# Kernel tuning notes

Measured on AMD Instinct MI355X. Metric: run time of the kernel, lower is better.

## Reference

```python
import jax, jax.numpy as jnp
import numpy as np

H, W = 32, 64          # img_size
NB = 4                 # fno_blocks
SCALE = 0.02


def setup_inputs() -> dict:
    key = jax.random.key(0)
    ks = jax.random.split(key, 8)
    B, N, C = 16, H * W, 768
    BS = C // NB
    x = jax.random.normal(ks[0], (B, N, C), dtype=jnp.float32)
    w1 = SCALE * jax.random.normal(ks[1], (2, NB, BS, BS), dtype=jnp.float32)
    b1 = SCALE * jax.random.normal(ks[2], (2, NB, BS), dtype=jnp.float32)
    w2 = SCALE * jax.random.normal(ks[3], (2, NB, BS, BS), dtype=jnp.float32)
    b2 = SCALE * jax.random.normal(ks[4], (2, NB, BS), dtype=jnp.float32)
    # Conv1d(C, C, kernel_size=1) == per-token linear layer over channels
    bias_w = jax.random.normal(ks[5], (C, C), dtype=jnp.float32) / np.sqrt(C)
    bias_b = jax.random.normal(ks[6], (C,), dtype=jnp.float32) * 0.01
    return {"x": x, "w1": w1, "b1": b1, "w2": w2, "b2": b2,
            "bias_w": bias_w, "bias_b": bias_b}


def _mul(a, w):
    # block-diagonal matmul: a [..., NB, BS], w [NB, BS, BS]
    return jnp.einsum('...bd,bdk->...bk', a, w)


def reference(x, w1, b1, w2, b2, bias_w, bias_b):
    B, N, C = x.shape
    BS = C // NB
    # Conv1d kernel-size-1 bias path
    bias = x @ bias_w.T + bias_b
    # spatial FFT
    xf = jnp.fft.rfftn(x.reshape(B, H, W, C), axes=(1, 2), norm='ortho')
    xf = xf.reshape(B, H, W // 2 + 1, NB, BS)
    xr, xi = xf.real, xf.imag
    # layer 1 (complex block-diag matmul + bias, ReLU on real/imag separately)
    r1 = jax.nn.relu(_mul(xr, w1[0]) - _mul(xi, w1[1]) + b1[0])
    i1 = jax.nn.relu(_mul(xr, w1[1]) + _mul(xi, w1[0]) + b1[1])
    # layer 2 -- NOTE: imag part uses the *updated* real part, matching the
    # original torch code's in-place reassignment order.
    r2 = _mul(r1, w2[0]) - _mul(i1, w2[1]) + b2[0]
    i2 = _mul(r2, w2[1]) + _mul(i1, w2[0]) + b2[1]
    xc = jax.lax.complex(r2, i2).reshape(B, H, W // 2 + 1, C)
    out = jnp.fft.irfftn(xc, s=(H, W), axes=(1, 2), norm='ortho')
    return out.reshape(B, N, C) + bias
```

## Files before the change

### kernel.cpp

```cpp
#include <hip/hip_runtime.h>
#include <hip/hip_bf16.h>
#include <stdint.h>

#define BB 16
#define HH 32
#define WW 64
#define CC 768
#define W2C 33
#define ROWW (2*CC)

typedef __bf16 bf16x8 __attribute__((ext_vector_type(8)));
typedef float f32x4 __attribute__((ext_vector_type(4)));

__device__ __forceinline__ unsigned short f2bf(float f) {
  __hip_bfloat16 h = __float2bfloat16(f);
  return __builtin_bit_cast(unsigned short, h);
}
__device__ __forceinline__ float bf2f(unsigned short u) {
  union { unsigned int i; float f; } x;
  x.i = ((unsigned int)u) << 16;
  return x.f;
}

__device__ __forceinline__ void g2l16(const void* g, void* l) {
  __builtin_amdgcn_global_load_lds((const __attribute__((address_space(1))) unsigned int*)g,
                                   (__attribute__((address_space(3))) unsigned int*)l,
                                   16, 0, 0);
}

#define WAITVM(n) asm volatile("s_waitcnt vmcnt(" #n ")" ::: "memory")
#define LGKM0() asm volatile("s_waitcnt lgkmcnt(0)" ::: "memory")
#define MEMFENCE() asm volatile("" ::: "memory")

__device__ __host__ constexpr int brevc(int x, int bits) {
  int r = 0;
  for (int i = 0; i < bits; ++i) r |= ((x >> i) & 1) << (bits - 1 - i);
  return r;
}

constexpr double TPI = 6.283185307179586476925286766559;
constexpr double tsin_(double x) {
  double t = x, s = x, x2 = x * x;
  for (int i = 1; i < 14; ++i) { t *= -x2 / (double)((2 * i) * (2 * i + 1)); s += t; }
  return s;
}
constexpr double tcos_(double x) {
  double t = 1.0, s = 1.0, x2 = x * x;
  for (int i = 1; i < 14; ++i) { t *= -x2 / (double)((2 * i - 1) * (2 * i)); s += t; }
  return s;
}
struct Tw64 { float c[64]; float s[64]; };
constexpr Tw64 mk_tw() {
  Tw64 r{};
  for (int k = 0; k < 64; ++k) {
    int q = k >> 4, m = k & 15;
    double a = (TPI / 64.0) * m;
    double cq = tcos_(a), sq = tsin_(a);
    double c, s;
    if (q == 0)      { c =  cq; s =  sq; }
    else if (q == 1) { c = -sq; s =  cq; }
    else if (q == 2) { c = -cq; s = -sq; }
    else             { c =  sq; s = -cq; }
    r.c[k] = (float)c;
    r.s[k] = (float)(-s);
  }
  return r;
}
constexpr Tw64 TW = mk_tw();

template<int N, bool INV>
__device__ __forceinline__ void fft_reg(float2 (&v)[N]) {
  constexpr int LOG2N = (N == 64) ? 6 : 5;
#pragma unroll
  for (int s = 0; s < LOG2N; ++s) {
    const int len = N >> s;
    const int half = len >> 1;
    const int tstep = 64 / len;
#pragma unroll
    for (int i = 0; i < N; i += len) {
#pragma unroll
      for (int j = 0; j < half; ++j) {
        float2 u = v[i + j];
        float2 t = v[i + j + half];
        float sr = u.x + t.x, si = u.y + t.y;
        float dr = u.x - t.x, di = u.y - t.y;
        float wr = TW.c[j * tstep];
        float wi = INV ? -TW.s[j * tstep] : TW.s[j * tstep];
        v[i + j] = make_float2(sr, si);
        v[i + j + half] = make_float2(dr * wr - di * wi, dr * wi + di * wr);
      }
    }
  }
}

__global__ __launch_bounds__(128) void fft_fwd_w(const float* __restrict__ x,
                                                 ushort2* __restrict__ yw) {
  __shared__ __align__(16) float xs[32][128];
  const int t = threadIdx.x;
  const int bh = blockIdx.x;
  const int c0 = blockIdx.y * 128;
  const float* xrow = x + (size_t)bh * (WW * CC) + c0;
  const int rg = t >> 5;
  const int lc = (t & 31) * 4;
  float2 v[32];
#pragma unroll
  for (int half = 0; half < 2; ++half) {
    if (half) __syncthreads();
    float4 f[8];
#pragma unroll
    for (int it = 0; it < 8; ++it)
      f[it] = *(const float4*)(xrow + (size_t)(half * 32 + it * 4 + rg) * CC + lc);
#pragma unroll
    for (int it = 0; it < 8; ++it)
      *(float4*)&xs[it * 4 + rg][lc] = f[it];
    __syncthreads();
#pragma unroll
    for (int n = 0; n < 16; ++n)
      v[half * 16 + n] = make_float2(xs[2 * n][t], xs[2 * n + 1][t]);
  }
  fft_reg<32, false>(v);
  ushort2* yp = yw + (size_t)bh * (W2C * CC) + c0 + t;
  {
    float2 Z0 = v[0];
    yp[0] = make_ushort2(f2bf(Z0.x + Z0.y), f2bf(0.f));
    yp[(size_t)32 * CC] = make_ushort2(f2bf(Z0.x - Z0.y), f2bf(0.f));
  }
#pragma unroll
  for (int k = 1; k < 32; ++k) {
    float2 Zk = v[brevc(k, 5)];
    float2 Zm = v[brevc(32 - k, 5)];
    float Er = 0.5f * (Zk.x + Zm.x), Ei = 0.5f * (Zk.y - Zm.y);
    float Odr = 0.5f * (Zk.y + Zm.y), Odi = -0.5f * (Zk.x - Zm.x);
    float wx = TW.c[k], wy = TW.s[k];
    float Xr = Er + wx * Odr - wy * Odi;
    float Xi = Ei + wx * Odi + wy * Odr;
    yp[(size_t)k * CC] = make_ushort2(f2bf(Xr), f2bf(Xi));
  }
}

__global__ __launch_bounds__(256) void fused_bias_ffth(
    const float* __restrict__ x, const unsigned short* __restrict__ bwb,
    const float* __restrict__ bb, unsigned short* __restrict__ biasout,
    const ushort2* __restrict__ yw, unsigned short* __restrict__ xf) {
  __shared__ __align__(16) unsigned short As[2][128 * 32];
  __shared__ __align__(16) unsigned short Bs[2][128 * 32];
  const int gid = blockIdx.x;
  bool isg; int idx;
  if (gid < 3072) { isg = (gid & 1) == 0; idx = gid >> 1; }
  else            { isg = false; idx = 1536 + (gid - 3072); }

  if (isg) {
    constexpr int K = 768, NT = 24, LDAF = 768;
    const int t = threadIdx.x;
    const int bx = idx & 255, by = idx >> 8;
    const size_t m0 = (size_t)bx * 128;
    const int n0 = by * 128;
    const float* Ap = x + m0 * LDAF;
    const unsigned short* Bp = bwb + (size_t)n0 * K;
    const int lane = t & 63, wave = t >> 6;
    const int lr = lane & 15, quad = lane >> 4;
    const int wm = (wave >> 1) * 64, wn = (wave & 1) * 64;
    const int row = t >> 2, sl = t & 3;
    const int kb = (sl ^ ((row >> 1) & 3)) * 8;
    const int swzf = (lr >> 1) & 3;
    f32x4 acc[4][4] = {};
    float4 a0, a1, a2, a3;

#define LDA4(k0_) do { \
    const float* ga_ = Ap + (size_t)row * LDAF + ((k0_) + kb); \
    a0 = *(const float4*)ga_; a1 = *(const float4*)(ga_ + 4); \
    const float* gc_ = ga_ + (size_t)64 * LDAF; \
    a2 = *(const float4*)gc_; a3 = *(const float4*)(gc_ + 4); \
  } while (0)
#define STB(k0_, s_) do { \
    const unsigned short* gb_ = Bp + (size_t)row * K + ((k0_) + kb); \
    g2l16(gb_, &Bs[s_][row * 32 + sl * 8]); \
    g2l16(gb_ + (size_t)64 * K, &Bs[s_][(row + 64) * 32 + sl * 8]); \
  } while (0)
#define WRA(s_) do { \
    union { bf16x8 v; unsigned short u[8]; } p0_, p1_; \
    p0_.u[0] = f2bf(a0.x); p0_.u[1] = f2bf(a0.y); p0_.u[2] = f2bf(a0.z); p0_.u[3] = f2bf(a0.w); \
    p0_.u[4] = f2bf(a1.x); p0_.u[5] = f2bf(a1.y); p0_.u[6] = f2bf(a1.z); p0_.u[7] = f2bf(a1.w); \
    p1_.u[0] = f2bf(a2.x); p1_.u[1] = f2bf(a2.y); p1_.u[2] = f2bf(a2.z); p1_.u[3] = f2bf(a2.w); \
    p1_.u[4] = f2bf(a3.x); p1_.u[5] = f2bf(a3.y); p1_.u[6] = f2bf(a3.z); p1_.u[7] = f2bf(a3.w); \
    *(bf16x8*)&As[s_][row * 32 + sl * 8] = p0_.v; \
    *(bf16x8*)&As[s_][(row + 64) * 32 + sl * 8] = p1_.v; \
  } while (0)

    LDA4(0); STB(0, 0);
    WRA(0);
    WAITVM(0); LGKM0();
    MEMFENCE(); __builtin_amdgcn_s_barrier(); MEMFENCE();
    int cur = 0;
    for (int tt = 0; tt < NT; ++tt) {
      if (tt + 1 < NT) { LDA4((tt + 1) * 32); STB((tt + 1) * 32, cur ^ 1); }
      bf16x8 af[4], bfr[4];
#pragma unroll
      for (int mi = 0; mi < 4; ++mi)
        af[mi] = *(const bf16x8*)&As[cur][(wm + mi * 16 + lr) * 32 + ((quad ^ swzf) * 8)];
#pragma unroll
      for (int ni = 0; ni < 4; ++ni)
        bfr[ni] = *(const bf16x8*)&Bs[cur][(wn + ni * 16 + lr) * 32 + ((quad ^ swzf) * 8)];
      __builtin_amdgcn_s_setprio(1);
#pragma unroll
      for (int mi = 0; mi < 4; ++mi)
#pragma unroll
        for (int ni = 0; ni < 4; ++ni)
          acc[mi][ni] = __builtin_amdgcn_mfma_f32_16x16x32_bf16(af[mi], bfr[ni], acc[mi][ni], 0, 0, 0);
      __builtin_amdgcn_s_setprio(0);
      if (tt + 1 < NT) {
        WRA(cur ^ 1);
        WAITVM(0); LGKM0();
        MEMFENCE(); __builtin_amdgcn_s_barrier(); MEMFENCE();
        cur ^= 1;
      }
    }
#undef LDA4
#undef STB
#undef WRA

#pragma unroll
    for (int mi = 0; mi < 4; ++mi) {
      const size_t mrow = m0 + wm + mi * 16 + quad * 4;
#pragma unroll
      for (int ni = 0; ni < 4; ++ni) {
        const int ncol = n0 + wn + ni * 16 + lr;
        const float bv = bb[ncol];
#pragma unroll
        for (int r = 0; r < 4; ++r)
          biasout[(mrow + r) * (size_t)768 + ncol] = f2bf(acc[mi][ni][r] + bv);
      }
    }
  } else {
    const int bk = idx - (idx / 528) * 528;
    const int cy = idx / 528;
    const int b = bk / W2C, kw = bk - b * W2C;
    const int c = cy * 256 + threadIdx.x;
    const ushort2* yp = yw + ((size_t)b * HH * W2C + kw) * CC + c;
    float2 v[32];
#pragma unroll
    for (int h = 0; h < 32; ++h) {
      ushort2 u = yp[(size_t)h * (W2C * CC)];
      v[h] = make_float2(bf2f(u.x), bf2f(u.y));
    }
    fft_reg<32, false>(v);
    const int nb = c / 192, cc = c - nb * 192;
    ushort2* xp = (ushort2*)(xf + (size_t)nb * 384 + 2 * cc);
    const float s = 0.022097086912079608f;
#pragma unroll
    for (int kh = 0; kh < 32; ++kh) {
      float2 z = v[brevc(kh, 5)];
      size_t m = ((size_t)b * HH + kh) * W2C + kw;
      xp[m * (ROWW / 2)] = make_ushort2(f2bf(z.x * s), f2bf(z.y * s));
    }
  }
}

__global__ __launch_bounds__(256) void fft_inv_h(const unsigned short* __restrict__ r2,
                                                 ushort2* __restrict__ g) {
  const int bk = blockIdx.x;
  const int b = bk / W2C, kw = bk - b * W2C;
  const int c = blockIdx.y * 256 + threadIdx.x;
  const int nb = c / 192, cc = c - nb * 192;
  const ushort2* rp = (const ushort2*)(r2 + (size_t)nb * 384 + 2 * cc);
  float2 v[32];
#pragma unroll
  for (int kh = 0; kh < 32; ++kh) {
    size_t m = ((size_t)b * HH + kh) * W2C + kw;
    ushort2 u = rp[m * (ROWW / 2)];
    v[kh] = make_float2(bf2f(u.x), bf2f(u.y));
  }
  fft_reg<32, true>(v);
  ushort2* gp = g + ((size_t)b * HH * W2C + kw) * CC + c;
#pragma unroll
  for (int h = 0; h < 32; ++h) {
    float2 z = v[brevc(h, 5)];
    gp[(size_t)h * (W2C * CC)] = make_ushort2(f2bf(z.x), f2bf(z.y));
  }
}

__global__ __launch_bounds__(128) void fft_inv_w(const ushort2* __restrict__ g,
                                                 const unsigned short* __restrict__ biasb,
                                                 float* __restrict__ out) {
  __shared__ __align__(16) float ys[32][128];
  const int t = threadIdx.x;
  const int bh = blockIdx.x;
  const int c0 = blockIdx.y * 128;
  const ushort2* gp = g + (size_t)bh * (W2C * CC) + c0 + t;
  float2 v[32];
  {
    float X0 = bf2f(gp[0].x);
    float X32 = bf2f(gp[(size_t)32 * CC].x);
    v[0] = make_float2(0.5f * (X0 + X32), 0.5f * (X0 - X32));
  }
#pragma unroll
  for (int k = 1; k < 32; ++k) {
    ushort2 uk = gp[(size_t)k * CC];
    ushort2 um = gp[(size_t)(32 - k) * CC];
    float2 Xk = make_float2(bf2f(uk.x), bf2f(uk.y));
    float2 Xm = make_float2(bf2f(um.x), bf2f(um.y));
    float Ar = 0.5f * (Xk.x + Xm.x), Ai = 0.5f * (Xk.y - Xm.y);
    float Dr = 0.5f * (Xk.x - Xm.x), Di = 0.5f * (Xk.y + Xm.y);
    float wx = TW.c[k], wy = TW.s[k];
    float Br = wx * Dr + wy * Di;
    float Bi = wx * Di - wy * Dr;
    v[k] = make_float2(Ar - Bi, Ai + Br);
  }
  fft_reg<32, true>(v);
  const float s2 = 0.04419417382415922f;
  float* orow = out + (size_t)bh * (WW * CC) + c0;
  const unsigned short* brow = biasb + (size_t)bh * (WW * CC) + c0;
  const int rg = t >> 5;
  const int lc = (t & 31) * 4;
#pragma unroll
  for (int half = 0; half < 2; ++half) {
    if (half) __syncthreads();
    ushort4 b4[8];
#pragma unroll
    for (int it = 0; it < 8; ++it)
      b4[it] = *(const ushort4*)(brow + (size_t)(half * 32 + it * 4 + rg) * CC + lc);
#pragma unroll
    for (int n = 0; n < 16; ++n) {
      float2 z = v[brevc(half * 16 + n, 5)];
      ys[2 * n][t] = z.x * s2;
      ys[2 * n + 1][t] = z.y * s2;
    }
    __syncthreads();
#pragma unroll
    for (int it = 0; it < 8; ++it) {
      const int w = half * 32 + it * 4 + rg;
      float4 f = *(const float4*)&ys[it * 4 + rg][lc];
      f.x += bf2f(b4[it].x); f.y += bf2f(b4[it].y);
      f.z += bf2f(b4[it].z); f.w += bf2f(b4[it].w);
      *(float4*)(orow + (size_t)w * CC + lc) = f;
    }
  }
}

template<bool RELU, bool OBF>
__global__ __launch_bounds__(256) void gemm_bt(
    const unsigned short* __restrict__ A, int lda, int aZ,
    const unsigned short* __restrict__ Bw, int K, int bZ,
    const float* __restrict__ bias, int biasZ,
    void* __restrict__ outp, int ldo, int oZ) {
  __shared__ __align__(16) unsigned short As[2][128 * 32];
  __shared__ __align__(16) unsigned short Bs[2][128 * 32];
  const int t = threadIdx.x;
  const int z = blockIdx.z;
  const size_t m0 = (size_t)blockIdx.x * 128;
  const int n0 = blockIdx.y * 128;
  const unsigned short* Ap = A + m0 * lda + (size_t)z * aZ;
  const unsigned short* Bp = Bw + (size_t)n0 * K + (size_t)z * bZ;
  const int lane = t & 63, wave = t >> 6;
  const int lr = lane & 15, quad = lane >> 4;
  const int wm = (wave >> 1) * 64, wn = (wave & 1) * 64;
  const int row = t >> 2;
  const int sl = t & 3;
  const int kb = (sl ^ ((row >> 1) & 3)) * 8;
  const int swzf = (lr >> 1) & 3;
  const int NT = K >> 5;
  f32x4 acc[4][4] = {};

#define STG(k0_, s_) do { \
    const unsigned short* ga_ = Ap + (size_t)row * lda + ((k0_) + kb); \
    g2l16(ga_, &As[s_][row * 32 + sl * 8]); \
    g2l16(ga_ + (size_t)64 * lda, &As[s_][(row + 64) * 32 + sl * 8]); \
    const unsigned short* gb_ = Bp + (size_t)row * K + ((k0_) + kb); \
    g2l16(gb_, &Bs[s_][row * 32 + sl * 8]); \
    g2l16(gb_ + (size_t)64 * K, &Bs[s_][(row + 64) * 32 + sl * 8]); \
  } while (0)

  STG(0, 0);
  WAITVM(0);
  MEMFENCE(); __builtin_amdgcn_s_barrier(); MEMFENCE();
  int cur = 0;
  for (int tt = 0; tt < NT; ++tt) {
    if (tt + 1 < NT) STG((tt + 1) * 32, cur ^ 1);
    bf16x8 af[4], bfr[4];
#pragma unroll
    for (int mi = 0; mi < 4; ++mi)
      af[mi] = *(const bf16x8*)&As[cur][(wm + mi * 16 + lr) * 32 + ((quad ^ swzf) * 8)];
#pragma unroll
    for (int ni = 0; ni < 4; ++ni)
      bfr[ni] = *(const bf16x8*)&Bs[cur][(wn + ni * 16 + lr) * 32 + ((quad ^ swzf) * 8)];
    __builtin_amdgcn_s_setprio(1);
#pragma unroll
    for (int mi = 0; mi < 4; ++mi)
#pragma unroll
      for (int ni = 0; ni < 4; ++ni)
        acc[mi][ni] = __builtin_amdgcn_mfma_f32_16x16x32_bf16(af[mi], bfr[ni], acc[mi][ni], 0, 0, 0);
    __builtin_amdgcn_s_setprio(0);
    if (tt + 1 < NT) {
      WAITVM(0);
      MEMFENCE(); __builtin_amdgcn_s_barrier(); MEMFENCE();
      cur ^= 1;
    }
  }
#undef STG

#pragma unroll
  for (int mi = 0; mi < 4; ++mi) {
    const size_t mrow = m0 + wm + mi * 16 + quad * 4;
#pragma unroll
    for (int ni = 0; ni < 4; ++ni) {
      const int ncol = n0 + wn + ni * 16 + lr;
      const float bv = bias[z * biasZ + ncol];
#pragma unroll
      for (int r = 0; r < 4; ++r) {
        float vv = acc[mi][ni][r] + bv;
        if (RELU) vv = fmaxf(vv, 0.f);
        const size_t off = (mrow + r) * (size_t)ldo + (size_t)z * oZ + ncol;
        if (OBF) ((unsigned short*)outp)[off] = f2bf(vv);
        else ((float*)outp)[off] = vv;
      }
    }
  }
}

__global__ __launch_bounds__(256) void prep_all(
    const float* __restrict__ bw, unsigned short* __restrict__ bwb,
    const float* __restrict__ w1, const float* __restrict__ b1,
    unsigned short* __restrict__ w1t, float* __restrict__ bias1,
    const float* __restrict__ w2, const float* __restrict__ b2,
    unsigned short* __restrict__ w2t, float* __restrict__ bias2) {
  const int gid = blockIdx.x;
  const int t = threadIdx.x;
  if (gid < 576) {
    const size_t i = ((size_t)gid * 256 + t) * 4;
    float4 v = *(const float4*)(bw + i);
    *(ushort4*)(bwb + i) = make_ushort4(f2bf(v.x), f2bf(v.y), f2bf(v.z), f2bf(v.w));
  } else if (gid < 576 + 2304) {
    const int idx = (gid - 576) * 256 + t;
    const int nb = idx / (384 * 384);
    const int rem = idx - nb * (384 * 384);
    const int n = rem / 384, k = rem - (rem / 384) * 384;
    const bool khi = k >= 192, nhi = n >= 192;
    const int kk = khi ? k - 192 : k, nn = nhi ? n - 192 : n;
    float val;
    if (!khi && !nhi)      val =  w1[((0 * 4 + nb) * 192 + kk) * 192 + nn];
    else if (khi && !nhi)  val = -w1[((1 * 4 + nb) * 192 + kk) * 192 + nn];
    else if (!khi && nhi)  val =  w1[((1 * 4 + nb) * 192 + kk) * 192 + nn];
    else                   val =  w1[((0 * 4 + nb) * 192 + kk) * 192 + nn];
    const int k2 = 2 * kk + (khi ? 1 : 0);
    const int n2 = 2 * nn + (nhi ? 1 : 0);
    w1t[((size_t)nb * 384 + n2) * 384 + k2] = f2bf(val);
    if (k == 0)
      bias1[nb * 384 + n2] = nhi ? b1[(1 * 4 + nb) * 192 + nn] : b1[(0 * 4 + nb) * 192 + nn];
  } else {
    const int idx = (gid - 2880) * 256 + t;
    const int nb = idx / (384 * 384);
    const int rem = idx - nb * (384 * 384);
    const int k = rem / 384, n = rem - (rem / 384) * 384;
    const bool khi = k >= 192, nhi = n >= 192;
    const int kk = khi ? k - 192 : k, nn = nhi ? n - 192 : n;
    float val;
    if (!khi && !nhi) {
      val = w2[((0 * 4 + nb) * 192 + kk) * 192 + nn];
    } else if (khi && !nhi) {
      val = -w2[((1 * 4 + nb) * 192 + kk) * 192 + nn];
    } else if (!khi && nhi) {
      float s = 0.f;
      for (int d = 0; d < 192; ++d)
        s += w2[((0 * 4 + nb) * 192 + kk) * 192 + d] * w2[((1 * 4 + nb) * 192 + d) * 192 + nn];
      val = s;
    } else {
      float s = 0.f;
      for (int d = 0; d < 192; ++d)
        s += w2[((1 * 4 + nb) * 192 + kk) * 192 + d] * w2[((1 * 4 + nb) * 192 + d) * 192 + nn];
      val = w2[((0 * 4 + nb) * 192 + kk) * 192 + nn] - s;
    }
    const int k2 = 2 * kk + (khi ? 1 : 0);
    const int n2 = 2 * nn + (nhi ? 1 : 0);
    w2t[((size_t)nb * 384 + n2) * 384 + k2] = f2bf(val);
    if (k == 0) {
      float bv;
      if (!nhi) {
        bv = b2[(0 * 4 + nb) * 192 + nn];
      } else {
        float s = 0.f;
        for (int d = 0; d < 192; ++d)
          s += b2[(0 * 4 + nb) * 192 + d] * w2[((1 * 4 + nb) * 192 + d) * 192 + nn];
        bv = b2[(1 * 4 + nb) * 192 + nn] + s;
      }
      bias2[nb * 384 + n2] = bv;
    }
  }
}

extern "C" void kernel_launch(void* const* d_in, const int* in_sizes, int n_in,
                              void* d_out, int out_size, void* d_ws, size_t ws_size,
                              hipStream_t stream) {
  (void)in_sizes; (void)n_in; (void)out_size; (void)ws_size;
  const float* x  = (const float*)d_in[0];
  const float* w1 = (const float*)d_in[1];
  const float* b1 = (const float*)d_in[2];
  const float* w2 = (const float*)d_in[3];
  const float* b2 = (const float*)d_in[4];
  const float* bw = (const float*)d_in[5];
  const float* bb = (const float*)d_in[6];
  float* out = (float*)d_out;

  char* p = (char*)d_ws;
  unsigned short* buf1 = (unsigned short*)p; p += 51904512;
  unsigned short* buf2 = (unsigned short*)p; p += 51904512;
  unsigned short* buf3 = (unsigned short*)p; p += 51904512;
  unsigned short* bwb  = (unsigned short*)p; p += 1179648;
  unsigned short* w1t  = (unsigned short*)p; p += 1179648;
  unsigned short* w2t  = (unsigned short*)p; p += 1179648;
  float* bias1 = (float*)p; p += 6144;
  float* bias2 = (float*)p; p += 6144;

  prep_all<<<5184, 256, 0, stream>>>(bw, bwb, w1, b1, w1t, bias1, w2, b2, w2t, bias2);
  fft_fwd_w<<<dim3(BB * HH, 6), 128, 0, stream>>>(x, (ushort2*)buf1);
  fused_bias_ffth<<<3120, 256, 0, stream>>>(x, bwb, bb, buf3, (const ushort2*)buf1, buf2);
  gemm_bt<true, true><<<dim3(132, 3, 4), 256, 0, stream>>>(
      buf2, ROWW, 384, w1t, 384, 384 * 384, bias1, 384, buf1, ROWW, 384);
  gemm_bt<false, true><<<dim3(132, 3, 4), 256, 0, stream>>>(
      buf1, ROWW, 384, w2t, 384, 384 * 384, bias2, 384, buf2, ROWW, 384);
  fft_inv_h<<<dim3(BB * W2C, 3), 256, 0, stream>>>(buf2, (ushort2*)buf1);
  fft_inv_w<<<dim3(BB * HH, 6), 128, 0, stream>>>((const ushort2*)buf1, buf3, out);
}
```

Baseline: 500.2 us.

## Unfuse bias GEMM from H-FFT and enlarge GEMM tiles to 256-wide

Splits the fused bias-GEMM/forward-H-FFT kernel back into two separate launches. It also grows the GEMM tiles: the spectral GEMMs now use 256x128 tiles (8x4 MFMA accumulators per wave) and the bias GEMM uses 128x256 tiles. The larger tiles cut redundant operand loads from global memory. The cost is higher register and LDS use per block, which lowers occupancy and leaves fewer blocks (e.g. 792 spectral-GEMM blocks instead of 1584). It also gives up the concurrency the fused kernel had between compute-bound GEMM blocks and memory-bound FFT blocks.

```diff
diff --git a/kernel.cpp b/kernel.cpp
--- a/kernel.cpp
+++ b/kernel.cpp
@@ -138,121 +138,27 @@
   }
 }
 
-__global__ __launch_bounds__(256) void fused_bias_ffth(
-    const float* __restrict__ x, const unsigned short* __restrict__ bwb,
-    const float* __restrict__ bb, unsigned short* __restrict__ biasout,
-    const ushort2* __restrict__ yw, unsigned short* __restrict__ xf) {
-  __shared__ __align__(16) unsigned short As[2][128 * 32];
-  __shared__ __align__(16) unsigned short Bs[2][128 * 32];
-  const int gid = blockIdx.x;
-  bool isg; int idx;
-  if (gid < 3072) { isg = (gid & 1) == 0; idx = gid >> 1; }
-  else            { isg = false; idx = 1536 + (gid - 3072); }
-
-  if (isg) {
-    constexpr int K = 768, NT = 24, LDAF = 768;
-    const int t = threadIdx.x;
-    const int bx = idx & 255, by = idx >> 8;
-    const size_t m0 = (size_t)bx * 128;
-    const int n0 = by * 128;
-    const float* Ap = x + m0 * LDAF;
-    const unsigned short* Bp = bwb + (size_t)n0 * K;
-    const int lane = t & 63, wave = t >> 6;
-    const int lr = lane & 15, quad = lane >> 4;
-    const int wm = (wave >> 1) * 64, wn = (wave & 1) * 64;
-    const int row = t >> 2, sl = t & 3;
-    const int kb = (sl ^ ((row >> 1) & 3)) * 8;
-    const int swzf = (lr >> 1) & 3;
-    f32x4 acc[4][4] = {};
-    float4 a0, a1, a2, a3;
-
-#define LDA4(k0_) do { \
-    const float* ga_ = Ap + (size_t)row * LDAF + ((k0_) + kb); \
-    a0 = *(const float4*)ga_; a1 = *(const float4*)(ga_ + 4); \
-    const float* gc_ = ga_ + (size_t)64 * LDAF; \
-    a2 = *(const float4*)gc_; a3 = *(const float4*)(gc_ + 4); \
-  } while (0)
-#define STB(k0_, s_) do { \
-    const unsigned short* gb_ = Bp + (size_t)row * K + ((k0_) + kb); \
-    g2l16(gb_, &Bs[s_][row * 32 + sl * 8]); \
-    g2l16(gb_ + (size_t)64 * K, &Bs[s_][(row + 64) * 32 + sl * 8]); \
-  } while (0)
-#define WRA(s_) do { \
-    union { bf16x8 v; unsigned short u[8]; } p0_, p1_; \
-    p0_.u[0] = f2bf(a0.x); p0_.u[1] = f2bf(a0.y); p0_.u[2] = f2bf(a0.z); p0_.u[3] = f2bf(a0.w); \
-    p0_.u[4] = f2bf(a1.x); p0_.u[5] = f2bf(a1.y); p0_.u[6] = f2bf(a1.z); p0_.u[7] = f2bf(a1.w); \
-    p1_.u[0] = f2bf(a2.x); p1_.u[1] = f2bf(a2.y); p1_.u[2] = f2bf(a2.z); p1_.u[3] = f2bf(a2.w); \
-    p1_.u[4] = f2bf(a3.x); p1_.u[5] = f2bf(a3.y); p1_.u[6] = f2bf(a3.z); p1_.u[7] = f2bf(a3.w); \
-    *(bf16x8*)&As[s_][row * 32 + sl * 8] = p0_.v; \
-    *(bf16x8*)&As[s_][(row + 64) * 32 + sl * 8] = p1_.v; \
-  } while (0)
-
-    LDA4(0); STB(0, 0);
-    WRA(0);
-    WAITVM(0); LGKM0();
-    MEMFENCE(); __builtin_amdgcn_s_barrier(); MEMFENCE();
-    int cur = 0;
-    for (int tt = 0; tt < NT; ++tt) {
-      if (tt + 1 < NT) { LDA4((tt + 1) * 32); STB((tt + 1) * 32, cur ^ 1); }
-      bf16x8 af[4], bfr[4];
-#pragma unroll
-      for (int mi = 0; mi < 4; ++mi)
-        af[mi] = *(const bf16x8*)&As[cur][(wm + mi * 16 + lr) * 32 + ((quad ^ swzf) * 8)];
-#pragma unroll
-      for (int ni = 0; ni < 4; ++ni)
-        bfr[ni] = *(const bf16x8*)&Bs[cur][(wn + ni * 16 + lr) * 32 + ((quad ^ swzf) * 8)];
-      __builtin_amdgcn_s_setprio(1);
-#pragma unroll
-      for (int mi = 0; mi < 4; ++mi)
-#pragma unroll
-        for (int ni = 0; ni < 4; ++ni)
-          acc[mi][ni] = __builtin_amdgcn_mfma_f32_16x16x32_bf16(af[mi], bfr[ni], acc[mi][ni], 0, 0, 0);
-      __builtin_amdgcn_s_setprio(0);
-      if (tt + 1 < NT) {
-        WRA(cur ^ 1);
-        WAITVM(0); LGKM0();
-        MEMFENCE(); __builtin_amdgcn_s_barrier(); MEMFENCE();
-        cur ^= 1;
-      }
-    }
-#undef LDA4
-#undef STB
-#undef WRA
-
-#pragma unroll
-    for (int mi = 0; mi < 4; ++mi) {
-      const size_t mrow = m0 + wm + mi * 16 + quad * 4;
-#pragma unroll
-      for (int ni = 0; ni < 4; ++ni) {
-        const int ncol = n0 + wn + ni * 16 + lr;
-        const float bv = bb[ncol];
-#pragma unroll
-        for (int r = 0; r < 4; ++r)
-          biasout[(mrow + r) * (size_t)768 + ncol] = f2bf(acc[mi][ni][r] + bv);
-      }
-    }
-  } else {
-    const int bk = idx - (idx / 528) * 528;
-    const int cy = idx / 528;
-    const int b = bk / W2C, kw = bk - b * W2C;
-    const int c = cy * 256 + threadIdx.x;
-    const ushort2* yp = yw + ((size_t)b * HH * W2C + kw) * CC + c;
-    float2 v[32];
-#pragma unroll
-    for (int h = 0; h < 32; ++h) {
-      ushort2 u = yp[(size_t)h * (W2C * CC)];
-      v[h] = make_float2(bf2f(u.x), bf2f(u.y));
-    }
-    fft_reg<32, false>(v);
-    const int nb = c / 192, cc = c - nb * 192;
-    ushort2* xp = (ushort2*)(xf + (size_t)nb * 384 + 2 * cc);
-    const float s = 0.022097086912079608f;
-#pragma unroll
-    for (int kh = 0; kh < 32; ++kh) {
-      float2 z = v[brevc(kh, 5)];
-      size_t m = ((size_t)b * HH + kh) * W2C + kw;
-      xp[m * (ROWW / 2)] = make_ushort2(f2bf(z.x * s), f2bf(z.y * s));
-    }
+__global__ __launch_bounds__(256) void fft_fwd_h(const ushort2* __restrict__ yw,
+                                                 unsigned short* __restrict__ xf) {
+  const int bk = blockIdx.x;
+  const int b = bk / W2C, kw = bk - b * W2C;
+  const int c = blockIdx.y * 256 + threadIdx.x;
+  const ushort2* yp = yw + ((size_t)b * HH * W2C + kw) * CC + c;
+  float2 v[32];
+#pragma unroll
+  for (int h = 0; h < 32; ++h) {
+    ushort2 u = yp[(size_t)h * (W2C * CC)];
+    v[h] = make_float2(bf2f(u.x), bf2f(u.y));
+  }
+  fft_reg<32, false>(v);
+  const int nb = c / 192, cc = c - nb * 192;
+  ushort2* xp = (ushort2*)(xf + (size_t)nb * 384 + 2 * cc);
+  const float s = 0.022097086912079608f;
+#pragma unroll
+  for (int kh = 0; kh < 32; ++kh) {
+    float2 z = v[brevc(kh, 5)];
+    size_t m = ((size_t)b * HH + kh) * W2C + kw;
+    xp[m * (ROWW / 2)] = make_ushort2(f2bf(z.x * s), f2bf(z.y * s));
   }
 }
 
@@ -337,34 +243,36 @@
   }
 }
 
-template<bool RELU, bool OBF>
-__global__ __launch_bounds__(256) void gemm_bt(
+template<bool RELU>
+__global__ __launch_bounds__(256) void gemm_spec(
     const unsigned short* __restrict__ A, int lda, int aZ,
     const unsigned short* __restrict__ Bw, int K, int bZ,
     const float* __restrict__ bias, int biasZ,
-    void* __restrict__ outp, int ldo, int oZ) {
-  __shared__ __align__(16) unsigned short As[2][128 * 32];
+    unsigned short* __restrict__ outp, int ldo, int oZ) {
+  __shared__ __align__(16) unsigned short As[2][256 * 32];
   __shared__ __align__(16) unsigned short Bs[2][128 * 32];
   const int t = threadIdx.x;
   const int z = blockIdx.z;
-  const size_t m0 = (size_t)blockIdx.x * 128;
+  const size_t m0 = (size_t)blockIdx.x * 256;
   const int n0 = blockIdx.y * 128;
   const unsigned short* Ap = A + m0 * lda + (size_t)z * aZ;
   const unsigned short* Bp = Bw + (size_t)n0 * K + (size_t)z * bZ;
   const int lane = t & 63, wave = t >> 6;
   const int lr = lane & 15, quad = lane >> 4;
-  const int wm = (wave >> 1) * 64, wn = (wave & 1) * 64;
+  const int wm = (wave >> 1) * 128, wn = (wave & 1) * 64;
   const int row = t >> 2;
   const int sl = t & 3;
   const int kb = (sl ^ ((row >> 1) & 3)) * 8;
   const int swzf = (lr >> 1) & 3;
   const int NT = K >> 5;
-  f32x4 acc[4][4] = {};
+  f32x4 acc[8][4] = {};
 
 #define STG(k0_, s_) do { \
     const unsigned short* ga_ = Ap + (size_t)row * lda + ((k0_) + kb); \
     g2l16(ga_, &As[s_][row * 32 + sl * 8]); \
     g2l16(ga_ + (size_t)64 * lda, &As[s_][(row + 64) * 32 + sl * 8]); \
+    g2l16(ga_ + (size_t)128 * lda, &As[s_][(row + 128) * 32 + sl * 8]); \
+    g2l16(ga_ + (size_t)192 * lda, &As[s_][(row + 192) * 32 + sl * 8]); \
     const unsigned short* gb_ = Bp + (size_t)row * K + ((k0_) + kb); \
     g2l16(gb_, &Bs[s_][row * 32 + sl * 8]); \
     g2l16(gb_ + (size_t)64 * K, &Bs[s_][(row + 64) * 32 + sl * 8]); \
@@ -376,16 +284,16 @@
   int cur = 0;
   for (int tt = 0; tt < NT; ++tt) {
     if (tt + 1 < NT) STG((tt + 1) * 32, cur ^ 1);
-    bf16x8 af[4], bfr[4];
-#pragma unroll
-    for (int mi = 0; mi < 4; ++mi)
+    bf16x8 af[8], bfr[4];
+#pragma unroll
+    for (int mi = 0; mi < 8; ++mi)
       af[mi] = *(const bf16x8*)&As[cur][(wm + mi * 16 + lr) * 32 + ((quad ^ swzf) * 8)];
 #pragma unroll
     for (int ni = 0; ni < 4; ++ni)
       bfr[ni] = *(const bf16x8*)&Bs[cur][(wn + ni * 16 + lr) * 32 + ((quad ^ swzf) * 8)];
     __builtin_amdgcn_s_setprio(1);
 #pragma unroll
-    for (int mi = 0; mi < 4; ++mi)
+    for (int mi = 0; mi < 8; ++mi)
 #pragma unroll
       for (int ni = 0; ni < 4; ++ni)
         acc[mi][ni] = __builtin_amdgcn_mfma_f32_16x16x32_bf16(af[mi], bfr[ni], acc[mi][ni], 0, 0, 0);
@@ -399,7 +307,7 @@
 #undef STG
 
 #pragma unroll
-  for (int mi = 0; mi < 4; ++mi) {
+  for (int mi = 0; mi < 8; ++mi) {
     const size_t mrow = m0 + wm + mi * 16 + quad * 4;
 #pragma unroll
     for (int ni = 0; ni < 4; ++ni) {
@@ -409,10 +317,99 @@
       for (int r = 0; r < 4; ++r) {
         float vv = acc[mi][ni][r] + bv;
         if (RELU) vv = fmaxf(vv, 0.f);
-        const size_t off = (mrow + r) * (size_t)ldo + (size_t)z * oZ + ncol;
-        if (OBF) ((unsigned short*)outp)[off] = f2bf(vv);
-        else ((float*)outp)[off] = vv;
+        outp[(mrow + r) * (size_t)ldo + (size_t)z * oZ + ncol] = f2bf(vv);
       }
+    }
+  }
+}
+
+__global__ __launch_bounds__(256) void gemm_bias(
+    const float* __restrict__ A,
+    const unsigned short* __restrict__ Bw,
+    const float* __restrict__ bias,
+    unsigned short* __restrict__ outp) {
+  constexpr int K = 768, NT = 24, LDAF = 768;
+  __shared__ __align__(16) unsigned short As[2][128 * 32];
+  __shared__ __align__(16) unsigned short Bs[2][256 * 32];
+  const int t = threadIdx.x;
+  const size_t m0 = (size_t)blockIdx.x * 128;
+  const int n0 = blockIdx.y * 256;
+  const float* Ap = A + m0 * LDAF;
+  const unsigned short* Bp = Bw + (size_t)n0 * K;
+  const int lane = t & 63, wave = t >> 6;
+  const int lr = lane & 15, quad = lane >> 4;
+  const int wm = (wave >> 1) * 64, wn = (wave & 1) * 128;
+  const int row = t >> 2, sl = t & 3;
+  const int kb = (sl ^ ((row >> 1) & 3)) * 8;
+  const int swzf = (lr >> 1) & 3;
+  f32x4 acc[4][8] = {};
+  float4 a0, a1, a2, a3;
+
+#define LDA4(k0_) do { \
+    const float* ga_ = Ap + (size_t)row * LDAF + ((k0_) + kb); \
+    a0 = *(const float4*)ga_; a1 = *(const float4*)(ga_ + 4); \
+    const float* gc_ = ga_ + (size_t)64 * LDAF; \
+    a2 = *(const float4*)gc_; a3 = *(const float4*)(gc_ + 4); \
+  } while (0)
+#define STB(k0_, s_) do { \
+    const unsigned short* gb_ = Bp + (size_t)row * K + ((k0_) + kb); \
+    g2l16(gb_, &Bs[s_][row * 32 + sl * 8]); \
+    g2l16(gb_ + (size_t)64 * K, &Bs[s_][(row + 64) * 32 + sl * 8]); \
+    g2l16(gb_ + (size_t)128 * K, &Bs[s_][(row + 128) * 32 + sl * 8]); \
+    g2l16(gb_ + (size_t)192 * K, &Bs[s_][(row + 192) * 32 + sl * 8]); \
+  } while (0)
+#define WRA(s_) do { \
+    union { bf16x8 v; unsigned short u[8]; } p0_, p1_; \
+    p0_.u[0] = f2bf(a0.x); p0_.u[1] = f2bf(a0.y); p0_.u[2] = f2bf(a0.z); p0_.u[3] = f2bf(a0.w); \
+    p0_.u[4] = f2bf(a1.x); p0_.u[5] = f2bf(a1.y); p0_.u[6] = f2bf(a1.z); p0_.u[7] = f2bf(a1.w); \
+    p1_.u[0] = f2bf(a2.x); p1_.u[1] = f2bf(a2.y); p1_.u[2] = f2bf(a2.z); p1_.u[3] = f2bf(a2.w); \
+    p1_.u[4] = f2bf(a3.x); p1_.u[5] = f2bf(a3.y); p1_.u[6] = f2bf(a3.z); p1_.u[7] = f2bf(a3.w); \
+    *(bf16x8*)&As[s_][row * 32 + sl * 8] = p0_.v; \
+    *(bf16x8*)&As[s_][(row + 64) * 32 + sl * 8] = p1_.v; \
+  } while (0)
+
+  LDA4(0); STB(0, 0);
+  WRA(0);
+  WAITVM(0); LGKM0();
+  MEMFENCE(); __builtin_amdgcn_s_barrier(); MEMFENCE();
+  int cur = 0;
+  for (int tt = 0; tt < NT; ++tt) {
+    if (tt + 1 < NT) { LDA4((tt + 1) * 32); STB((tt + 1) * 32, cur ^ 1); }
+    bf16x8 af[4], bfr[8];
+#pragma unroll
+    for (int mi = 0; mi < 4; ++mi)
+      af[mi] = *(const bf16x8*)&As[cur][(wm + mi * 16 + lr) * 32 + ((quad ^ swzf) * 8)];
+#pragma unroll
+    for (int ni = 0; ni < 8; ++ni)
+      bfr[ni] = *(const bf16x8*)&Bs[cur][(wn + ni * 16 + lr) * 32 + ((quad ^ swzf) * 8)];
+    __builtin_amdgcn_s_setprio(1);
+#pragma unroll
+    for (int mi = 0; mi < 4; ++mi)
+#pragma unroll
+      for (int ni = 0; ni < 8; ++ni)
+        acc[mi][ni] = __builtin_amdgcn_mfma_f32_16x16x32_bf16(af[mi], bfr[ni], acc[mi][ni], 0, 0, 0);
+    __builtin_amdgcn_s_setprio(0);
+    if (tt + 1 < NT) {
+      WRA(cur ^ 1);
+      WAITVM(0); LGKM0();
+      MEMFENCE(); __builtin_amdgcn_s_barrier(); MEMFENCE();
+      cur ^= 1;
+    }
+  }
+#undef LDA4
+#undef STB
+#undef WRA
+
+#pragma unroll
+  for (int mi = 0; mi < 4; ++mi) {
+    const size_t mrow = m0 + wm + mi * 16 + quad * 4;
+#pragma unroll
+    for (int ni = 0; ni < 8; ++ni) {
+      const int ncol = n0 + wn + ni * 16 + lr;
+      const float bv = bias[ncol];
+#pragma unroll
+      for (int r = 0; r < 4; ++r)
+        outp[(mrow + r) * (size_t)768 + ncol] = f2bf(acc[mi][ni][r] + bv);
     }
   }
 }
@@ -512,10 +509,11 @@
 
   prep_all<<<5184, 256, 0, stream>>>(bw, bwb, w1, b1, w1t, bias1, w2, b2, w2t, bias2);
   fft_fwd_w<<<dim3(BB * HH, 6), 128, 0, stream>>>(x, (ushort2*)buf1);
-  fused_bias_ffth<<<3120, 256, 0, stream>>>(x, bwb, bb, buf3, (const ushort2*)buf1, buf2);
-  gemm_bt<true, true><<<dim3(132, 3, 4), 256, 0, stream>>>(
+  gemm_bias<<<dim3(256, 3), 256, 0, stream>>>(x, bwb, bb, buf3);
+  fft_fwd_h<<<dim3(BB * W2C, 3), 256, 0, stream>>>((const ushort2*)buf1, buf2);
+  gemm_spec<true><<<dim3(66, 3, 4), 256, 0, stream>>>(
       buf2, ROWW, 384, w1t, 384, 384 * 384, bias1, 384, buf1, ROWW, 384);
-  gemm_bt<false, true><<<dim3(132, 3, 4), 256, 0, stream>>>(
+  gemm_spec<false><<<dim3(66, 3, 4), 256, 0, stream>>>(
       buf1, ROWW, 384, w2t, 384, 384 * 384, bias2, 384, buf2, ROWW, 384);
   fft_inv_h<<<dim3(BB * W2C, 3), 256, 0, stream>>>(buf2, (ushort2*)buf1);
   fft_inv_w<<<dim3(BB * HH, 6), 128, 0, stream>>>((const ushort2*)buf1, buf3, out);
```

Result: slower. 523.7 us (+4.7%).
